# Kernel optimization log

Measured on AMD Instinct MI355X. Metric: run time of the kernel, lower is better.

The kernel has to match this reference:

```python
import jax, jax.numpy as jnp
import numpy as np

N = 100000
F_IN = 128
HID = 256
NUM_CLASSES = 64
E = 1600000


def setup_inputs() -> dict:
    key = jax.random.key(0)
    ks = jax.random.split(key, 10)
    x = jax.random.normal(ks[0], (N, F_IN), dtype=jnp.float32)
    edge_index = jax.random.randint(ks[1], (2, E), 0, N, dtype=jnp.int32)
    edge_weight = jax.random.uniform(ks[2], (E,), dtype=jnp.float32)
    def glorot(k, shape):
        lim = np.sqrt(6.0 / (shape[0] + shape[1]))
        return jax.random.uniform(k, shape, jnp.float32, -lim, lim)
    W0 = glorot(ks[3], (F_IN, HID)); b0 = jnp.zeros((HID,), jnp.float32)
    W1 = glorot(ks[4], (HID, HID)); b1 = jnp.zeros((HID,), jnp.float32)
    W2 = glorot(ks[5], (HID, NUM_CLASSES)); b2 = jnp.zeros((NUM_CLASSES,), jnp.float32)
    return {"x": x, "edge_index": edge_index, "edge_weight": edge_weight,
            "W0": W0, "b0": b0, "W1": W1, "b1": b1, "W2": W2, "b2": b2}


def _gcn_norm(edge_index, edge_weight, n_nodes):
    # renormalization trick: add self-loops (weight 1), D^-1/2 A D^-1/2
    loop = jnp.arange(n_nodes, dtype=edge_index.dtype)
    src = jnp.concatenate([edge_index[0], loop])
    dst = jnp.concatenate([edge_index[1], loop])
    w = jnp.concatenate([edge_weight, jnp.ones((n_nodes,), edge_weight.dtype)])
    deg = jax.ops.segment_sum(w, dst, num_segments=n_nodes)
    d_inv_sqrt = jnp.where(deg > 0, jax.lax.rsqrt(jnp.maximum(deg, 1e-12)), 0.0)
    norm = d_inv_sqrt[src] * w * d_inv_sqrt[dst]
    return src, dst, norm


def _gcn_layer(x, src, dst, norm, W, b, act):
    h = x @ W                                  # [N, d_out] project first (cheap dense)
    msg = h[src] * norm[:, None]               # [E+N, d_out] gather + scale
    out = jax.ops.segment_sum(msg, dst, num_segments=x.shape[0]) + b
    return act(out) if act is not None else out


def reference(x, edge_index, edge_weight, W0, b0, W1, b1, W2, b2):
    n_nodes = x.shape[0]
    src, dst, norm = _gcn_norm(edge_index, edge_weight, n_nodes)
    # dropout is identity at inference (training=None)
    h = _gcn_layer(x, src, dst, norm, W0, b0, jax.nn.relu)
    h = _gcn_layer(h, src, dst, norm, W1, b1, jax.nn.relu)
    h = _gcn_layer(h, src, dst, norm, W2, b2, None)
    return h
```

## Files before the change

kernel.cpp:

```cpp
#include <hip/hip_runtime.h>

#define N_NODES 100000
#define F_IN 128
#define HID 256
#define NCLS 64
#define N_EDGES 1600000

typedef _Float16 f16;
typedef f16 half8 __attribute__((ext_vector_type(8)));
typedef f16 half4 __attribute__((ext_vector_type(4)));
typedef float f32x4 __attribute__((ext_vector_type(4)));

#define FIXED_SCALE 67108864.0f

__global__ void k_init(unsigned long long* __restrict__ degp, int n) {
    int i = blockIdx.x * 256 + threadIdx.x;
    if (i < n) degp[i] = (unsigned long long)(1u << 26);
}

__global__ void k_deg(const int* __restrict__ dst, const float* __restrict__ w,
                      unsigned long long* __restrict__ degp, int e) {
    int i = blockIdx.x * 256 + threadIdx.x;
    if (i < e) {
        unsigned long long c = (1ULL << 40) |
            (unsigned long long)__float2uint_rn(w[i] * FIXED_SCALE);
        atomicAdd(&degp[dst[i]], c);
    }
}

__global__ void k_dis(const unsigned long long* __restrict__ degp,
                      float* __restrict__ dis, float* __restrict__ selfnorm,
                      int* __restrict__ cnt, int n) {
    int i = blockIdx.x * 256 + threadIdx.x;
    if (i < n) {
        unsigned long long p = degp[i];
        int c = (int)(p >> 40);
        float deg = (float)(p & ((1ULL << 40) - 1)) * (1.0f / FIXED_SCALE);
        float d = rsqrtf(deg);
        dis[i] = d;
        selfnorm[i] = d * d;
        cnt[i] = c;
    }
}

__global__ void k_scan1(const int* __restrict__ cnt, int* __restrict__ incl,
                        int* __restrict__ bsum, int n) {
    __shared__ int s[256];
    int t = threadIdx.x;
    int i = blockIdx.x * 256 + t;
    int v = (i < n) ? cnt[i] : 0;
    s[t] = v;
    __syncthreads();
    #pragma unroll
    for (int off = 1; off < 256; off <<= 1) {
        int x = (t >= off) ? s[t - off] : 0;
        __syncthreads();
        s[t] += x;
        __syncthreads();
    }
    if (i < n) incl[i] = s[t];
    if (t == 255) bsum[blockIdx.x] = s[255];
}

__global__ void k_scan2(const int* __restrict__ bsum, int* __restrict__ boff, int nb) {
    __shared__ int s[512];
    int t = threadIdx.x;
    int v = (t < nb) ? bsum[t] : 0;
    s[t] = v;
    __syncthreads();
    #pragma unroll
    for (int off = 1; off < 512; off <<= 1) {
        int x = (t >= off) ? s[t - off] : 0;
        __syncthreads();
        s[t] += x;
        __syncthreads();
    }
    if (t < nb) boff[t] = s[t] - v;
}

__global__ void k_scan3(int* __restrict__ row, const int* __restrict__ cnt,
                        const int* __restrict__ boff, int n) {
    int i = blockIdx.x * 256 + threadIdx.x;
    if (i < n) row[i] = row[i] - cnt[i] + boff[i >> 8];
}

__global__ void k_scatter(const int* __restrict__ src, const int* __restrict__ dst,
                          const float* __restrict__ w, const float* __restrict__ dis,
                          int* __restrict__ row, int2* __restrict__ csr, int e) {
    int i = blockIdx.x * 256 + threadIdx.x;
    if (i < e) {
        int s = src[i], d = dst[i];
        float nw = dis[s] * w[i] * dis[d];
        int pos = atomicAdd(&row[d], 1);
        csr[pos] = make_int2(s, __float_as_int(nw));
    }
}

__global__ void k_f32_to_f16(const float* __restrict__ src, f16* __restrict__ dst, int n4) {
    int i = blockIdx.x * 256 + threadIdx.x;
    if (i < n4) {
        float4 v = *(const float4*)&src[(size_t)i * 4];
        half4 o;
        o[0] = (f16)v.x; o[1] = (f16)v.y; o[2] = (f16)v.z; o[3] = (f16)v.w;
        *(half4*)&dst[(size_t)i * 4] = o;
    }
}

__global__ void k_wt(const float* __restrict__ W, f16* __restrict__ Wt, int K, int D) {
    int i = blockIdx.x * 256 + threadIdx.x;
    if (i < K * D) {
        int k = i / D, d = i % D;
        Wt[d * K + k] = (f16)W[i];
    }
}

template <int K, int DOUT, bool BIAS_RELU>
__global__ __launch_bounds__(256) void gemm_mfma(const f16* __restrict__ in,
                                                 const f16* __restrict__ Wt,
                                                 const float* __restrict__ bias,
                                                 f16* __restrict__ out,
                                                 int nNodes) {
    constexpr int BM = 128, BN = 64, BK = 32;
    constexpr int AP = 40;
    constexpr int CP = 72;
    constexpr int SMEM = (BM * AP + BN * AP) > (BM * CP) ? (BM * AP + BN * AP) : (BM * CP);
    __shared__ f16 smem[SMEM];
    f16* As = smem;
    f16* Bs = smem + BM * AP;

    const int t = threadIdx.x;
    const int w = t >> 6;
    const int lane = t & 63;
    const int quad = lane >> 4;
    const int l16 = lane & 15;
    const int nodeBase = blockIdx.x * BM;
    const int colBase = blockIdx.y * BN;

    f32x4 acc[2][4] = {};

    for (int k0 = 0; k0 < K; k0 += BK) {
        {
            int koff = (t & 3) * 8;
            #pragma unroll
            for (int p = 0; p < 2; ++p) {
                int r = (t >> 2) + p * 64;
                int gn = nodeBase + r;
                if (gn >= nNodes) gn = nNodes - 1;
                half8 v = *(const half8*)&in[(size_t)gn * K + k0 + koff];
                *(half8*)&As[r * AP + koff] = v;
            }
        }
        {
            int koff = (t & 3) * 8;
            int c = t >> 2;
            half8 v = *(const half8*)&Wt[(size_t)(colBase + c) * K + k0 + koff];
            *(half8*)&Bs[c * AP + koff] = v;
        }
        __syncthreads();

        half8 a[2];
        #pragma unroll
        for (int rt = 0; rt < 2; ++rt)
            a[rt] = *(const half8*)&As[(w * 32 + rt * 16 + l16) * AP + quad * 8];
        #pragma unroll
        for (int ct = 0; ct < 4; ++ct) {
            half8 b = *(const half8*)&Bs[(ct * 16 + l16) * AP + quad * 8];
            acc[0][ct] = __builtin_amdgcn_mfma_f32_16x16x32_f16(a[0], b, acc[0][ct], 0, 0, 0);
            acc[1][ct] = __builtin_amdgcn_mfma_f32_16x16x32_f16(a[1], b, acc[1][ct], 0, 0, 0);
        }
        __syncthreads();
    }

    float bv[4];
    #pragma unroll
    for (int ct = 0; ct < 4; ++ct)
        bv[ct] = BIAS_RELU ? bias[colBase + ct * 16 + l16] : 0.0f;

    f16* Cs = smem;
    #pragma unroll
    for (int rt = 0; rt < 2; ++rt)
        #pragma unroll
        for (int ct = 0; ct < 4; ++ct)
            #pragma unroll
            for (int r = 0; r < 4; ++r) {
                int rr = w * 32 + rt * 16 + quad * 4 + r;
                int cc = ct * 16 + l16;
                float v = acc[rt][ct][r];
                if (BIAS_RELU) v = fmaxf(v + bv[ct], 0.0f);
                Cs[rr * CP + cc] = (f16)v;
            }
    __syncthreads();
    #pragma unroll
    for (int p = 0; p < 4; ++p) {
        int r = (t >> 3) + p * 32;
        int gn = nodeBase + r;
        int chunk = (t & 7) * 8;
        if (gn < nNodes)
            *(half8*)&out[(size_t)gn * DOUT + colBase + chunk] =
                *(const half8*)&Cs[r * CP + chunk];
    }
}

template <int DOUT, int TPN, bool HAS_BIAS, bool OUT_F32>
__global__ __launch_bounds__(256) void agg_csr(const f16* __restrict__ h,
                                               const int2* __restrict__ csr,
                                               const int* __restrict__ row,
                                               const int* __restrict__ cnt,
                                               const float* __restrict__ sn,
                                               const float* __restrict__ bias,
                                               void* __restrict__ outv, int nNodes) {
    constexpr int NPB = 256 / TPN;
    int node = blockIdx.x * NPB + threadIdx.x / TPN;
    if (node >= nNodes) return;
    int lane = threadIdx.x % TPN;
    int col = lane * 8;

    float s = sn[node];
    half8 hv = *(const half8*)&h[(size_t)node * DOUT + col];
    float acc[8];
    #pragma unroll
    for (int i = 0; i < 8; ++i)
        acc[i] = s * (float)hv[i] + (HAS_BIAS ? bias[col + i] : 0.0f);

    int end = row[node];
    int e = end - cnt[node];
    for (; e + 1 < end; e += 2) {
        int2 e0 = csr[e], e1 = csr[e + 1];
        float w0 = __int_as_float(e0.y), w1 = __int_as_float(e1.y);
        half8 a0 = *(const half8*)&h[(size_t)e0.x * DOUT + col];
        half8 a1 = *(const half8*)&h[(size_t)e1.x * DOUT + col];
        #pragma unroll
        for (int i = 0; i < 8; ++i) acc[i] += w0 * (float)a0[i] + w1 * (float)a1[i];
    }
    if (e < end) {
        int2 e0 = csr[e];
        float w0 = __int_as_float(e0.y);
        half8 a0 = *(const half8*)&h[(size_t)e0.x * DOUT + col];
        #pragma unroll
        for (int i = 0; i < 8; ++i) acc[i] += w0 * (float)a0[i];
    }

    if (OUT_F32) {
        float* out = (float*)outv;
        float4 r0 = make_float4(acc[0], acc[1], acc[2], acc[3]);
        float4 r1 = make_float4(acc[4], acc[5], acc[6], acc[7]);
        *(float4*)&out[(size_t)node * DOUT + col] = r0;
        *(float4*)&out[(size_t)node * DOUT + col + 4] = r1;
    } else {
        f16* out = (f16*)outv;
        half8 o;
        #pragma unroll
        for (int i = 0; i < 8; ++i) o[i] = (f16)acc[i];
        *(half8*)&out[(size_t)node * DOUT + col] = o;
    }
}

extern "C" void kernel_launch(void* const* d_in, const int* in_sizes, int n_in,
                              void* d_out, int out_size, void* d_ws, size_t ws_size,
                              hipStream_t stream) {
    const float* x  = (const float*)d_in[0];
    const int*   ei = (const int*)d_in[1];
    const float* ew = (const float*)d_in[2];
    const float* W0 = (const float*)d_in[3];
    const float* b0 = (const float*)d_in[4];
    const float* W1 = (const float*)d_in[5];
    const float* b1 = (const float*)d_in[6];
    const float* W2 = (const float*)d_in[7];
    const float* b2 = (const float*)d_in[8];
    const int* src = ei;
    const int* dst = ei + N_EDGES;
    float* outp = (float*)d_out;

    char* ws = (char*)d_ws;
    unsigned long long* degp = (unsigned long long*)ws;  ws += N_NODES * 8;
    float* dis      = (float*)ws;  ws += N_NODES * 4;
    float* selfnorm = (float*)ws;  ws += N_NODES * 4;
    int*   cnt      = (int*)ws;    ws += N_NODES * 4;
    int*   row      = (int*)ws;    ws += N_NODES * 4;
    int*   bsum     = (int*)ws;    ws += 512 * 4;
    int*   boff     = (int*)ws;    ws += 512 * 4;
    int2*  csr      = (int2*)ws;   ws += (size_t)N_EDGES * 8;
    f16*   xh       = (f16*)ws;    ws += (size_t)N_NODES * F_IN * 2;
    f16*   Wt0      = (f16*)ws;    ws += F_IN * HID * 2;
    f16*   Wt1      = (f16*)ws;    ws += HID * HID * 2;
    f16*   Wt2      = (f16*)ws;    ws += HID * NCLS * 2;
    f16*   bufA     = (f16*)ws;    ws += (size_t)N_NODES * HID * 2;
    f16*   bufB     = (f16*)ws;    ws += (size_t)N_NODES * HID * 2;

    const int nb = (N_NODES + 255) / 256;
    const int eb = (N_EDGES + 255) / 256;

    k_init<<<nb, 256, 0, stream>>>(degp, N_NODES);
    k_deg<<<eb, 256, 0, stream>>>(dst, ew, degp, N_EDGES);
    k_dis<<<nb, 256, 0, stream>>>(degp, dis, selfnorm, cnt, N_NODES);
    k_scan1<<<nb, 256, 0, stream>>>(cnt, row, bsum, N_NODES);
    k_scan2<<<1, 512, 0, stream>>>(bsum, boff, nb);
    k_scan3<<<nb, 256, 0, stream>>>(row, cnt, boff, N_NODES);
    k_scatter<<<eb, 256, 0, stream>>>(src, dst, ew, dis, row, csr, N_EDGES);

    k_f32_to_f16<<<(N_NODES * (F_IN / 4) + 255) / 256, 256, 0, stream>>>(x, xh, N_NODES * (F_IN / 4));
    k_wt<<<(F_IN * HID + 255) / 256, 256, 0, stream>>>(W0, Wt0, F_IN, HID);
    k_wt<<<(HID * HID + 255) / 256, 256, 0, stream>>>(W1, Wt1, HID, HID);
    k_wt<<<(HID * NCLS + 255) / 256, 256, 0, stream>>>(W2, Wt2, HID, NCLS);

    const int gX = (N_NODES + 127) / 128;

    agg_csr<F_IN, 16, false, false><<<(N_NODES + 15) / 16, 256, 0, stream>>>(
        xh, csr, row, cnt, selfnorm, nullptr, bufA, N_NODES);
    gemm_mfma<F_IN, HID, true><<<dim3(gX, HID / 64), 256, 0, stream>>>(bufA, Wt0, b0, bufB, N_NODES);

    agg_csr<HID, 32, false, false><<<(N_NODES + 7) / 8, 256, 0, stream>>>(
        bufB, csr, row, cnt, selfnorm, nullptr, bufA, N_NODES);
    gemm_mfma<HID, HID, true><<<dim3(gX, HID / 64), 256, 0, stream>>>(bufA, Wt1, b1, bufB, N_NODES);

    gemm_mfma<HID, NCLS, false><<<dim3(gX, NCLS / 64), 256, 0, stream>>>(bufB, Wt2, nullptr, bufA, N_NODES);
    agg_csr<NCLS, 8, true, true><<<(N_NODES + 31) / 32, 256, 0, stream>>>(
        bufA, csr, row, cnt, selfnorm, b2, outp, N_NODES);
}
```

Baseline: 598.7 us.

## Record per-edge slot from degree atomic and fuse preprocessing into one kernel

The degree atomic now returns the old packed count, which gives each edge its slot within its destination's CSR segment. This removes the second atomicAdd pass in the scatter kernel, which becomes a plain indexed write. The x-to-fp16 conversion and the three weight transposes are merged into the same launch as the degree pass, cutting kernel launches. In exchange it adds a 1.6M-int seq buffer with its own write and read traffic, and the row array now holds exclusive start offsets, so the aggregation reads start plus count.

```diff
diff --git a/kernel.cpp b/kernel.cpp
--- a/kernel.cpp
+++ b/kernel.cpp
@@ -18,13 +18,48 @@
     if (i < n) degp[i] = (unsigned long long)(1u << 26);
 }
 
-__global__ void k_deg(const int* __restrict__ dst, const float* __restrict__ w,
-                      unsigned long long* __restrict__ degp, int e) {
-    int i = blockIdx.x * 256 + threadIdx.x;
-    if (i < e) {
-        unsigned long long c = (1ULL << 40) |
-            (unsigned long long)__float2uint_rn(w[i] * FIXED_SCALE);
-        atomicAdd(&degp[dst[i]], c);
+#define EB   6250
+#define XB   12500
+#define W0B  128
+#define W1B  256
+#define W2B  64
+__global__ __launch_bounds__(256) void mega1(
+        const int* __restrict__ dst, const float* __restrict__ ew,
+        unsigned long long* __restrict__ degp, int* __restrict__ seq,
+        const float* __restrict__ x, f16* __restrict__ xh,
+        const float* __restrict__ W0, f16* __restrict__ Wt0,
+        const float* __restrict__ W1, f16* __restrict__ Wt1,
+        const float* __restrict__ W2, f16* __restrict__ Wt2) {
+    int bid = blockIdx.x;
+    int t = threadIdx.x;
+    if (bid < EB) {
+        int i = bid * 256 + t;
+        if (i < N_EDGES) {
+            unsigned long long c = (1ULL << 40) |
+                (unsigned long long)__float2uint_rn(ew[i] * FIXED_SCALE);
+            unsigned long long old = atomicAdd(&degp[dst[i]], c);
+            seq[i] = (int)(old >> 40);
+        }
+    } else if (bid < EB + XB) {
+        int i = (bid - EB) * 256 + t;
+        if (i < N_NODES * (F_IN / 4)) {
+            float4 v = *(const float4*)&x[(size_t)i * 4];
+            half4 o;
+            o[0] = (f16)v.x; o[1] = (f16)v.y; o[2] = (f16)v.z; o[3] = (f16)v.w;
+            *(half4*)&xh[(size_t)i * 4] = o;
+        }
+    } else if (bid < EB + XB + W0B) {
+        int i = (bid - EB - XB) * 256 + t;
+        int k = i / HID, d = i % HID;
+        Wt0[d * F_IN + k] = (f16)W0[i];
+    } else if (bid < EB + XB + W0B + W1B) {
+        int i = (bid - EB - XB - W0B) * 256 + t;
+        int k = i / HID, d = i % HID;
+        Wt1[d * HID + k] = (f16)W1[i];
+    } else {
+        int i = (bid - EB - XB - W0B - W1B) * 256 + t;
+        int k = i / NCLS, d = i % NCLS;
+        Wt2[d * HID + k] = (f16)W2[i];
     }
 }
 
@@ -34,12 +69,11 @@
     int i = blockIdx.x * 256 + threadIdx.x;
     if (i < n) {
         unsigned long long p = degp[i];
-        int c = (int)(p >> 40);
+        cnt[i] = (int)(p >> 40);
         float deg = (float)(p & ((1ULL << 40) - 1)) * (1.0f / FIXED_SCALE);
         float d = rsqrtf(deg);
         dis[i] = d;
         selfnorm[i] = d * d;
-        cnt[i] = c;
     }
 }
 
@@ -84,33 +118,16 @@
     if (i < n) row[i] = row[i] - cnt[i] + boff[i >> 8];
 }
 
-__global__ void k_scatter(const int* __restrict__ src, const int* __restrict__ dst,
-                          const float* __restrict__ w, const float* __restrict__ dis,
-                          int* __restrict__ row, int2* __restrict__ csr, int e) {
+__global__ void k_place(const int* __restrict__ src, const int* __restrict__ dst,
+                        const float* __restrict__ w, const int* __restrict__ seq,
+                        const int* __restrict__ row, const float* __restrict__ dis,
+                        int2* __restrict__ csr, int e) {
     int i = blockIdx.x * 256 + threadIdx.x;
     if (i < e) {
         int s = src[i], d = dst[i];
         float nw = dis[s] * w[i] * dis[d];
-        int pos = atomicAdd(&row[d], 1);
+        int pos = row[d] + seq[i];
         csr[pos] = make_int2(s, __float_as_int(nw));
-    }
-}
-
-__global__ void k_f32_to_f16(const float* __restrict__ src, f16* __restrict__ dst, int n4) {
-    int i = blockIdx.x * 256 + threadIdx.x;
-    if (i < n4) {
-        float4 v = *(const float4*)&src[(size_t)i * 4];
-        half4 o;
-        o[0] = (f16)v.x; o[1] = (f16)v.y; o[2] = (f16)v.z; o[3] = (f16)v.w;
-        *(half4*)&dst[(size_t)i * 4] = o;
-    }
-}
-
-__global__ void k_wt(const float* __restrict__ W, f16* __restrict__ Wt, int K, int D) {
-    int i = blockIdx.x * 256 + threadIdx.x;
-    if (i < K * D) {
-        int k = i / D, d = i % D;
-        Wt[d * K + k] = (f16)W[i];
     }
 }
 
@@ -222,8 +239,8 @@
     for (int i = 0; i < 8; ++i)
         acc[i] = s * (float)hv[i] + (HAS_BIAS ? bias[col + i] : 0.0f);
 
-    int end = row[node];
-    int e = end - cnt[node];
+    int e = row[node];
+    int end = e + cnt[node];
     for (; e + 1 < end; e += 2) {
         int2 e0 = csr[e], e1 = csr[e + 1];
         float w0 = __int_as_float(e0.y), w1 = __int_as_float(e1.y);
@@ -273,13 +290,14 @@
 
     char* ws = (char*)d_ws;
     unsigned long long* degp = (unsigned long long*)ws;  ws += N_NODES * 8;
+    int2*  csr      = (int2*)ws;   ws += (size_t)N_EDGES * 8;
+    int*   seq      = (int*)ws;    ws += (size_t)N_EDGES * 4;
     float* dis      = (float*)ws;  ws += N_NODES * 4;
     float* selfnorm = (float*)ws;  ws += N_NODES * 4;
     int*   cnt      = (int*)ws;    ws += N_NODES * 4;
     int*   row      = (int*)ws;    ws += N_NODES * 4;
     int*   bsum     = (int*)ws;    ws += 512 * 4;
     int*   boff     = (int*)ws;    ws += 512 * 4;
-    int2*  csr      = (int2*)ws;   ws += (size_t)N_EDGES * 8;
     f16*   xh       = (f16*)ws;    ws += (size_t)N_NODES * F_IN * 2;
     f16*   Wt0      = (f16*)ws;    ws += F_IN * HID * 2;
     f16*   Wt1      = (f16*)ws;    ws += HID * HID * 2;
@@ -291,17 +309,13 @@
     const int eb = (N_EDGES + 255) / 256;
 
     k_init<<<nb, 256, 0, stream>>>(degp, N_NODES);
-    k_deg<<<eb, 256, 0, stream>>>(dst, ew, degp, N_EDGES);
+    mega1<<<EB + XB + W0B + W1B + W2B, 256, 0, stream>>>(
+        dst, ew, degp, seq, x, xh, W0, Wt0, W1, Wt1, W2, Wt2);
     k_dis<<<nb, 256, 0, stream>>>(degp, dis, selfnorm, cnt, N_NODES);
     k_scan1<<<nb, 256, 0, stream>>>(cnt, row, bsum, N_NODES);
     k_scan2<<<1, 512, 0, stream>>>(bsum, boff, nb);
     k_scan3<<<nb, 256, 0, stream>>>(row, cnt, boff, N_NODES);
-    k_scatter<<<eb, 256, 0, stream>>>(src, dst, ew, dis, row, csr, N_EDGES);
-
-    k_f32_to_f16<<<(N_NODES * (F_IN / 4) + 255) / 256, 256, 0, stream>>>(x, xh, N_NODES * (F_IN / 4));
-    k_wt<<<(F_IN * HID + 255) / 256, 256, 0, stream>>>(W0, Wt0, F_IN, HID);
-    k_wt<<<(HID * HID + 255) / 256, 256, 0, stream>>>(W1, Wt1, HID, HID);
-    k_wt<<<(HID * NCLS + 255) / 256, 256, 0, stream>>>(W2, Wt2, HID, NCLS);
+    k_place<<<eb, 256, 0, stream>>>(src, dst, ew, seq, row, dis, csr, N_EDGES);
 
     const int gX = (N_NODES + 127) / 128;
 
```

Result: faster. 553.0 us (-7.6%).
